# Kernel tuning notes

Measured on AMD Instinct MI355X. Metric: run time of the kernel, lower is better.

The kernel has to match this reference:

```python
import jax, jax.numpy as jnp
import numpy as np

MAX_LENGTH = 25
SOS_TOKEN = 0


def setup_inputs() -> dict:
    key = jax.random.key(0)
    B, S, H, V = 32, 50, 256, 50257
    ks = jax.random.split(key, 16)
    u = lambda k, shape, fan: jax.random.uniform(k, shape, jnp.float32, -1.0, 1.0) / np.sqrt(fan)
    return {
        "encoder_hidden": jax.random.normal(ks[0], (1, B, H), jnp.float32),
        "encoder_outputs": jax.random.normal(ks[1], (B, S, H), jnp.float32),
        "target_tensor": jax.random.randint(ks[2], (B, MAX_LENGTH), 0, V),
        "embedding": jax.random.normal(ks[3], (V, H), jnp.float32) * 0.02,
        "Wa_w": u(ks[4], (H, H), H), "Wa_b": u(ks[5], (H,), H),
        "Ua_w": u(ks[6], (H, H), H), "Ua_b": u(ks[7], (H,), H),
        "Va_w": u(ks[8], (1, H), H), "Va_b": u(ks[9], (1,), H),
        "gru_w_ih": u(ks[10], (3 * H, 2 * H), H), "gru_b_ih": u(ks[11], (3 * H,), H),
        "gru_w_hh": u(ks[12], (3 * H, H), H), "gru_b_hh": u(ks[13], (3 * H,), H),
        "out_w": u(ks[14], (V, H), H), "out_b": u(ks[15], (V,), H),
    }


def reference(encoder_hidden, encoder_outputs, target_tensor, embedding,
              Wa_w, Wa_b, Ua_w, Ua_b, Va_w, Va_b,
              gru_w_ih, gru_b_ih, gru_w_hh, gru_b_hh, out_w, out_b):
    B, S, H = encoder_outputs.shape
    keys = encoder_outputs
    # Ua(keys) is step-invariant: precompute.  [B,S,H]
    ua_keys = jnp.einsum("bsh,gh->bsg", keys, Ua_w) + Ua_b
    # teacher-forced input tokens: [SOS, target[:, :-1]] -> [T,B]
    toks = jnp.concatenate(
        [jnp.full((B, 1), SOS_TOKEN, dtype=target_tensor.dtype),
         target_tensor[:, : MAX_LENGTH - 1]], axis=1).T

    def step(h, tok):
        # h: [B,H], tok: [B]
        emb = embedding[tok]                                   # [B,H]
        # Bahdanau attention (dropout is identity in eval mode)
        wa_q = h @ Wa_w.T + Wa_b                               # [B,H]
        e = jnp.tanh(wa_q[:, None, :] + ua_keys)               # [B,S,H]
        scores = jnp.einsum("bsh,h->bs", e, Va_w[0]) + Va_b[0]  # [B,S]
        w = jax.nn.softmax(scores, axis=-1)                    # [B,S]
        ctx = jnp.einsum("bs,bsh->bh", w, keys)                # [B,H]
        # GRU cell (PyTorch gate order: r, z, n)
        x = jnp.concatenate([emb, ctx], axis=-1)               # [B,2H]
        gi = x @ gru_w_ih.T + gru_b_ih                         # [B,3H]
        gh = h @ gru_w_hh.T + gru_b_hh                         # [B,3H]
        ir, iz, inn = jnp.split(gi, 3, axis=-1)
        hr, hz, hn = jnp.split(gh, 3, axis=-1)
        r = jax.nn.sigmoid(ir + hr)
        z = jax.nn.sigmoid(iz + hz)
        n = jnp.tanh(inn + r * hn)
        h2 = (1.0 - z) * n + z * h
        logits = h2 @ out_w.T + out_b                          # [B,V]
        return h2, (logits, w)

    h0 = encoder_hidden[0]                                     # [B,H]
    hT, (logits, attn) = jax.lax.scan(step, h0, toks)          # [T,B,V], [T,B,S]
    dec_out = jax.nn.log_softmax(logits.transpose(1, 0, 2), axis=-1)  # [B,T,V]
    attentions = attn.transpose(1, 0, 2)                       # [B,T,S]
    return dec_out, hT[None], attentions
```

## Files before the change

kernel.cpp:

```cpp
#include <hip/hip_runtime.h>
#include <math.h>

#define B_ 32
#define S_ 50
#define H_ 256
#define T_ 25
#define V_ 50257
#define VP 50260
#define NCH 786
#define NROW (B_ * T_)
#define NWROW 1024
#define VT_ 3144
#define MROW 54
#define SOS 0

typedef unsigned short ushort_t;
typedef __attribute__((ext_vector_type(8))) unsigned short ushort8;
typedef __attribute__((ext_vector_type(8))) short short8v;
typedef __attribute__((ext_vector_type(4))) float f32x4;

__device__ ushort_t g_ua[B_ * S_ * H_];
__device__ ushort_t g_hbf[NROW * H_];
__device__ float    g_gie[T_ * B_ * 3 * H_];
__device__ ushort_t g_wpk[(size_t)VT_ * 32 * 16 * 8];
__device__ ushort_t g_wcat[NWROW * H_];
__device__ ushort_t g_MT2[B_ * 768 * MROW];
__device__ ushort_t g_lgt[(size_t)NROW * VP];
__device__ float    g_pmax[NROW * NCH];
__device__ float    g_psum[NROW * NCH];

__device__ __forceinline__ float bf2f(ushort_t h) {
  union { unsigned int u; float f; } c; c.u = ((unsigned int)h) << 16; return c.f;
}
__device__ __forceinline__ ushort_t f2bf(float f) {
  union { float f; unsigned int u; } c; c.f = f;
  unsigned int u = c.u;
  return (ushort_t)((u + 0x7FFFu + ((u >> 16) & 1u)) >> 16);
}
__device__ __forceinline__ float tanh_fast(float x) {
  const float e = __expf(2.f * x);
  return 1.f - 2.f / (e + 1.f);
}

__global__ void k_pre(const float* __restrict__ keys, const float* __restrict__ Ua_w,
                      const float* __restrict__ Ua_b, const float* __restrict__ Wa_b,
                      const float* __restrict__ W_hh, const float* __restrict__ Wa_w,
                      const float* __restrict__ W_ih, const float* __restrict__ b_ih,
                      const int* __restrict__ tgt, const float* __restrict__ emb_tab) {
  __shared__ float sbuf[S_ * H_];
  const int bid = blockIdx.x, tid = threadIdx.x;

  if (bid < B_ * S_) {
    sbuf[tid] = keys[bid * H_ + tid];
    sbuf[H_ + tid] = Ua_b[tid] + Wa_b[tid];
    __syncthreads();
    const int sub = tid & 15, grp = tid >> 4;
#pragma unroll 4
    for (int it = 0; it < 16; ++it) {
      const int row = it * 16 + grp;
      const float4* wr = (const float4*)(Ua_w + (size_t)row * H_);
      float a = 0.f;
#pragma unroll
      for (int st = 0; st < 4; ++st) {
        const float4 w = wr[st * 16 + sub];
        const float4 x = *(const float4*)(sbuf + st * 64 + sub * 4);
        a += w.x * x.x + w.y * x.y + w.z * x.z + w.w * x.w;
      }
      a += __shfl_xor(a, 8); a += __shfl_xor(a, 4);
      a += __shfl_xor(a, 2); a += __shfl_xor(a, 1);
      if (sub == 0) g_ua[(size_t)bid * H_ + row] = f2bf(a + sbuf[H_ + row]);
    }
  } else if (bid < 1984) {
    const int cc = bid - 1600;
    const int c = cc % 12, b = cc / 12;
    {
      const float4* src = (const float4*)(keys + (size_t)b * S_ * H_);
      float4* dst = (float4*)sbuf;
      for (int i = tid; i < S_ * H_ / 4; i += 256) dst[i] = src[i];
    }
    __syncthreads();
    const int sub = tid & 15, grp = tid >> 4;
#pragma unroll 1
    for (int it = 0; it < 4; ++it) {
      const int j = c * 64 + it * 16 + grp;
      float w16[16];
#pragma unroll
      for (int kp = 0; kp < 16; ++kp)
        w16[kp] = W_ih[(size_t)j * (2 * H_) + H_ + sub + 16 * kp];
#pragma unroll 1
      for (int s = 0; s < S_; ++s) {
        float a = 0.f;
#pragma unroll
        for (int kp = 0; kp < 16; ++kp) a += w16[kp] * sbuf[s * H_ + sub + 16 * kp];
        a += __shfl_xor(a, 8); a += __shfl_xor(a, 4);
        a += __shfl_xor(a, 2); a += __shfl_xor(a, 1);
        if (sub == 0) g_MT2[(size_t)b * 768 * MROW + j * MROW + s] = f2bf(a);
      }
    }
  } else if (bid < 2284) {
    const int cc = bid - 1984;
    const int chunk = cc % 12, t = cc / 12;
    for (int i = tid; i < B_ * H_; i += 256) {
      const int b = i >> 8, g = i & 255;
      const int tok = (t == 0) ? SOS : tgt[b * T_ + (t - 1)];
      sbuf[i] = emb_tab[(size_t)tok * H_ + g];
    }
    __syncthreads();
    const int vl = tid & 63, wd = tid >> 6;
    const int j = chunk * 64 + vl;
    const float4* wrow = (const float4*)(W_ih + (size_t)j * (2 * H_));
    const float4* se4 = (const float4*)sbuf;
    float acc[8];
    const float base = b_ih[j];
#pragma unroll
    for (int bb = 0; bb < 8; ++bb) acc[bb] = base;
    for (int k4 = 0; k4 < 64; ++k4) {
      const float4 w = wrow[k4];
#pragma unroll
      for (int bb = 0; bb < 8; ++bb) {
        const float4 x = se4[(wd * 8 + bb) * 64 + k4];
        acc[bb] += w.x * x.x + w.y * x.y + w.z * x.z + w.w * x.w;
      }
    }
#pragma unroll
    for (int bb = 0; bb < 8; ++bb)
      g_gie[((size_t)t * B_ + (wd * 8 + bb)) * (3 * H_) + j] = acc[bb];
  } else {
    const size_t i0 = (size_t)(bid - 2284) * 256 + tid;
    for (size_t i = i0; i < (size_t)NWROW * H_; i += 256u * 256u) {
      const int r = (int)(i >> 8), k = (int)(i & 255);
      const float v = (r < 256) ? Wa_w[r * H_ + k] : W_hh[(r - 256) * H_ + k];
      g_wcat[i] = f2bf(v);
    }
  }
}

__global__ void __launch_bounds__(1024, 1)
k_recur(const float* __restrict__ enc_h, const float* __restrict__ Va_w,
        const float* __restrict__ Va_b, const float* __restrict__ b_hh,
        const float* __restrict__ out_w, float* __restrict__ out) {
  __shared__ ushort_t s_ua[S_ * H_];
  __shared__ ushort_t s_M[768 * MROW];
  __shared__ float s_res[NWROW];
  __shared__ float s_mw[768];
  __shared__ float s_h[H_];
  __shared__ float s_va[H_];
  __shared__ float s_score[64], s_w[64];
  const int bidx = blockIdx.x, tid = threadIdx.x;

  if (bidx >= 32) {
    const size_t total = (size_t)VT_ * 32 * 16;
    for (size_t p = (size_t)(bidx - 32) * 1024 + tid; p < total;
         p += (size_t)(gridDim.x - 32) * 1024) {
      const int c = (int)(p & 15);
      const int kg = (int)((p >> 4) & 31);
      const int vt = (int)(p >> 9);
      const int v = vt * 16 + c;
      short8v val = {0, 0, 0, 0, 0, 0, 0, 0};
      if (v < V_) {
        const float4* owr = (const float4*)(out_w + (size_t)v * H_ + kg * 8);
        const float4 f0 = owr[0], f1 = owr[1];
        val[0] = (short)f2bf(f0.x); val[1] = (short)f2bf(f0.y);
        val[2] = (short)f2bf(f0.z); val[3] = (short)f2bf(f0.w);
        val[4] = (short)f2bf(f1.x); val[5] = (short)f2bf(f1.y);
        val[6] = (short)f2bf(f1.z); val[7] = (short)f2bf(f1.w);
      }
      ((short8v*)g_wpk)[p] = val;
    }
    return;
  }

  const int b = bidx;
  const int lane = tid & 63, wid = tid >> 6;
  const int sub = lane & 15;
  const int grp = tid >> 4;

  {
    const uint4* src = (const uint4*)(g_ua + (size_t)b * S_ * H_);
    uint4* dst = (uint4*)s_ua;
    for (int i = tid; i < S_ * H_ / 8; i += 1024) dst[i] = src[i];
    const uint4* src2 = (const uint4*)(g_MT2 + (size_t)b * 768 * MROW);
    uint4* dst2 = (uint4*)s_M;
    for (int i = tid; i < 768 * MROW / 8; i += 1024) dst2[i] = src2[i];
  }
  float hreg = 0.f, bhh0 = 0.f, bhh1 = 0.f, bhh2 = 0.f;
  if (tid < H_) {
    hreg = enc_h[b * H_ + tid];
    s_h[tid] = hreg;
    s_va[tid] = Va_w[tid];
    bhh0 = b_hh[tid]; bhh1 = b_hh[H_ + tid]; bhh2 = b_hh[2 * H_ + tid];
  }
  if (tid >= 50 && tid < 64) s_w[tid] = 0.f;
  const float vab = Va_b[0];
  __syncthreads();

  for (int t = 0; t < T_; ++t) {
    float gie0 = 0.f, gie1 = 0.f, gie2 = 0.f;
    if (tid < H_) {
      const float* gp = g_gie + ((size_t)t * B_ + b) * (3 * H_);
      gie0 = gp[tid]; gie1 = gp[H_ + tid]; gie2 = gp[2 * H_ + tid];
    }

#pragma unroll 4
    for (int it = 0; it < 16; ++it) {
      const int row = it * 64 + grp;
      const ushort8* wr = (const ushort8*)(g_wcat + (size_t)row * H_);
      const ushort8 w0 = wr[sub], w1 = wr[16 + sub];
      const float* v0 = s_h + sub * 8;
      const float* v1 = s_h + 128 + sub * 8;
      float a0 = 0.f, a1 = 0.f;
#pragma unroll
      for (int j = 0; j < 8; ++j) { a0 += bf2f(w0[j]) * v0[j]; a1 += bf2f(w1[j]) * v1[j]; }
      float a = a0 + a1;
      a += __shfl_xor(a, 8); a += __shfl_xor(a, 4);
      a += __shfl_xor(a, 2); a += __shfl_xor(a, 1);
      if (sub == 0) s_res[row] = a;
    }
    __syncthreads();

    for (int s = wid; s < S_; s += 16) {
      const ushort_t* uarow = s_ua + s * H_;
      float acc = 0.f;
#pragma unroll
      for (int i = 0; i < 4; ++i) {
        const int gg = lane + i * 64;
        acc += tanh_fast(s_res[gg] + bf2f(uarow[gg])) * s_va[gg];
      }
      for (int off = 32; off > 0; off >>= 1) acc += __shfl_xor(acc, off);
      if (lane == 0) s_score[s] = acc + vab;
    }
    __syncthreads();

    if (tid < 64) {
      const float v = (tid < S_) ? s_score[tid] : -INFINITY;
      float m = v;
      for (int off = 32; off > 0; off >>= 1) m = fmaxf(m, __shfl_xor(m, off));
      const float e = (tid < S_) ? __expf(v - m) : 0.f;
      float ssum = e;
      for (int off = 32; off > 0; off >>= 1) ssum += __shfl_xor(ssum, off);
      const float w = e / ssum;
      if (tid < S_) {
        s_w[tid] = w;
        out[(size_t)B_ * T_ * V_ + (size_t)B_ * H_ + (size_t)(b * T_ + t) * S_ + tid] = w;
      }
    }
    __syncthreads();

    if (tid < 768) {
      const unsigned int* m32 = (const unsigned int*)s_M + tid * (MROW / 2);
      float acc = 0.f;
#pragma unroll
      for (int i = 0; i < 25; ++i) {
        const unsigned int mv = m32[i];
        acc += bf2f((ushort_t)(mv & 0xffffu)) * s_w[2 * i];
        acc += bf2f((ushort_t)(mv >> 16)) * s_w[2 * i + 1];
      }
      s_mw[tid] = acc;
    }
    __syncthreads();

    if (tid < H_) {
      const float gi0 = gie0 + s_mw[tid];
      const float gi1 = gie1 + s_mw[H_ + tid];
      const float gi2 = gie2 + s_mw[2 * H_ + tid];
      const float gh0 = s_res[256 + tid] + bhh0;
      const float gh1 = s_res[512 + tid] + bhh1;
      const float gh2 = s_res[768 + tid] + bhh2;
      const float r = 1.f / (1.f + __expf(-(gi0 + gh0)));
      const float z = 1.f / (1.f + __expf(-(gi1 + gh1)));
      const float n = tanh_fast(gi2 + r * gh2);
      const float h2 = (1.f - z) * n + z * hreg;
      hreg = h2;
      s_h[tid] = h2;
      g_hbf[((size_t)b * T_ + t) * H_ + tid] = f2bf(h2);
      if (t == T_ - 1) out[(size_t)B_ * T_ * V_ + b * H_ + tid] = h2;
    }
    __syncthreads();
  }
}

__global__ void __launch_bounds__(512, 1)
k_logits(const float* __restrict__ out_b) {
  __shared__ ushort_t sA[128 * 256];
  __shared__ ushort_t sB[128 * 256];
  const int tid = threadIdx.x, nb = blockIdx.x;
  const int n0 = nb * 128;
  const int lane = tid & 63, wv = tid >> 6;
  const int wm = wv >> 1, wn = wv & 1;
  const int l16 = lane & 15, l4 = lane >> 4;

  {
    const short8v* src = (const short8v*)g_wpk + (size_t)nb * 4096;
    short8v* dst = (short8v*)sB;
    for (int i = tid; i < 4096; i += 512) dst[i] = src[i];
  }

  int vcol[4]; float bias[4]; bool valid[4];
#pragma unroll
  for (int ni = 0; ni < 4; ++ni) {
    vcol[ni] = n0 + wn * 64 + ni * 16 + l16;
    valid[ni] = (vcol[ni] < V_);
    bias[ni] = valid[ni] ? out_b[vcol[ni]] : 0.f;
  }
  const int chunk = nb * 2 + wn;

#pragma unroll 1
  for (int mt = 0; mt < 7; ++mt) {
    const int m0 = mt * 128;
    __syncthreads();
    for (int i = tid; i < 128 * 32; i += 512) {
      const int row = i >> 5, ks = i & 31;
      const int m = m0 + row;
      ushort8 val;
      if (m < NROW) val = ((const ushort8*)(g_hbf + (size_t)m * H_))[ks];
      else { ushort8 z = {0, 0, 0, 0, 0, 0, 0, 0}; val = z; }
      *(ushort8*)((char*)sA + row * 512 + ((ks ^ (row & 7)) << 4)) = val;
    }
    __syncthreads();

    f32x4 acc[2][4];
#pragma unroll
    for (int mi = 0; mi < 2; ++mi)
#pragma unroll
      for (int ni = 0; ni < 4; ++ni) acc[mi][ni] = (f32x4){0.f, 0.f, 0.f, 0.f};

#pragma unroll 1
    for (int kk = 0; kk < 8; ++kk) {
      short8v a[2], bfr[4];
#pragma unroll
      for (int mi = 0; mi < 2; ++mi) {
        const int row = wm * 32 + mi * 16 + l16;
        const int ks = kk * 4 + l4;
        a[mi] = *(const short8v*)((const char*)sA + row * 512 + ((ks ^ (row & 7)) << 4));
      }
#pragma unroll
      for (int ni = 0; ni < 4; ++ni)
        bfr[ni] = ((const short8v*)sB)[(((wn * 4 + ni) * 32) + kk * 4 + l4) * 16 + l16];
#pragma unroll
      for (int mi = 0; mi < 2; ++mi)
#pragma unroll
        for (int ni = 0; ni < 4; ++ni)
          acc[mi][ni] = __builtin_amdgcn_mfma_f32_16x16x32_bf16(a[mi], bfr[ni], acc[mi][ni], 0, 0, 0);
    }

#pragma unroll
    for (int mi = 0; mi < 2; ++mi) {
#pragma unroll
      for (int j = 0; j < 4; ++j) {
        const int m = m0 + wm * 32 + mi * 16 + l4 * 4 + j;
        float vv[4];
        float mx = -INFINITY;
#pragma unroll
        for (int ni = 0; ni < 4; ++ni) {
          vv[ni] = acc[mi][ni][j] + bias[ni];
          if (valid[ni]) mx = fmaxf(mx, vv[ni]);
        }
        mx = fmaxf(mx, __shfl_xor(mx, 1)); mx = fmaxf(mx, __shfl_xor(mx, 2));
        mx = fmaxf(mx, __shfl_xor(mx, 4)); mx = fmaxf(mx, __shfl_xor(mx, 8));
        float es = 0.f;
#pragma unroll
        for (int ni = 0; ni < 4; ++ni) if (valid[ni]) es += __expf(vv[ni] - mx);
        es += __shfl_xor(es, 1); es += __shfl_xor(es, 2);
        es += __shfl_xor(es, 4); es += __shfl_xor(es, 8);
        if (m < NROW) {
#pragma unroll
          for (int ni = 0; ni < 4; ++ni)
            if (valid[ni]) g_lgt[(size_t)m * VP + vcol[ni]] = f2bf(vv[ni]);
          if (l16 == 0) {
            g_pmax[(size_t)m * NCH + chunk] = mx;
            g_psum[(size_t)m * NCH + chunk] = es;
          }
        }
      }
    }
  }
}

__global__ void k_wlse(float* __restrict__ out) {
  __shared__ float red[4];
  const int r = blockIdx.x;
  const int tid = threadIdx.x;
  float m = -INFINITY;
  for (int i = tid; i < NCH; i += 256) m = fmaxf(m, g_pmax[(size_t)r * NCH + i]);
  for (int off = 32; off > 0; off >>= 1) m = fmaxf(m, __shfl_xor(m, off));
  if ((tid & 63) == 0) red[tid >> 6] = m;
  __syncthreads();
  m = fmaxf(fmaxf(red[0], red[1]), fmaxf(red[2], red[3]));
  __syncthreads();
  float s = 0.f;
  for (int i = tid; i < NCH; i += 256)
    s += g_psum[(size_t)r * NCH + i] * __expf(g_pmax[(size_t)r * NCH + i] - m);
  for (int off = 32; off > 0; off >>= 1) s += __shfl_xor(s, off);
  if ((tid & 63) == 0) red[tid >> 6] = s;
  __syncthreads();
  s = red[0] + red[1] + red[2] + red[3];
  float lse = m + logf(s);
  if (!isfinite(lse)) lse = 0.f;
  const size_t obase = (size_t)r * V_;
  const unsigned int* row32 = (const unsigned int*)(g_lgt + (size_t)r * VP);
#pragma unroll 1
  for (int i = tid; i < V_ / 2; i += 256) {
    const unsigned int u = row32[i];
    out[obase + 2 * i]     = bf2f((ushort_t)(u & 0xffffu)) - lse;
    out[obase + 2 * i + 1] = bf2f((ushort_t)(u >> 16)) - lse;
  }
  if (tid == 0)
    out[obase + V_ - 1] = bf2f(g_lgt[(size_t)r * VP + V_ - 1]) - lse;
}

extern "C" void kernel_launch(void* const* d_in, const int* in_sizes, int n_in,
                              void* d_out, int out_size, void* d_ws, size_t ws_size,
                              hipStream_t stream) {
  const float* enc_h  = (const float*)d_in[0];
  const float* keys   = (const float*)d_in[1];
  const int*   tgt    = (const int*)d_in[2];
  const float* emb    = (const float*)d_in[3];
  const float* Wa_w   = (const float*)d_in[4];
  const float* Wa_b   = (const float*)d_in[5];
  const float* Ua_w   = (const float*)d_in[6];
  const float* Ua_b   = (const float*)d_in[7];
  const float* Va_w   = (const float*)d_in[8];
  const float* Va_b   = (const float*)d_in[9];
  const float* W_ih   = (const float*)d_in[10];
  const float* b_ih   = (const float*)d_in[11];
  const float* W_hh   = (const float*)d_in[12];
  const float* b_hh   = (const float*)d_in[13];
  const float* out_w  = (const float*)d_in[14];
  const float* out_b  = (const float*)d_in[15];
  float* out = (float*)d_out;
  (void)d_ws; (void)ws_size;

  hipLaunchKernelGGL(k_pre, dim3(2540), dim3(256), 0, stream,
                     keys, Ua_w, Ua_b, Wa_b, W_hh, Wa_w, W_ih, b_ih, tgt, emb);
  hipLaunchKernelGGL(k_recur, dim3(32 + 1792), dim3(1024), 0, stream,
                     enc_h, Va_w, Va_b, b_hh, out_w, out);
  hipLaunchKernelGGL(k_logits, dim3(393), dim3(512), 0, stream, out_b);
  hipLaunchKernelGGL(k_wlse, dim3(NROW), dim3(256), 0, stream, out);
}
```

Measured before the change: 493.7 us.

## Compute Ua(keys) projection with bf16 MFMA tiled GEMM in preprocessing kernel

Replaces the per-row scalar dot-product blocks (1600 blocks) for the Ua(keys) projection with 26 blocks that each compute a 128x128 tile using bf16 MFMA 16x16x32. Keys are staged in LDS with an XOR swizzle and the Ua weights are converted to bf16 on the fly. The intent is to cut the cost and block count of the preprocessing kernel. Inputs are now rounded to bf16 before the multiply, so accuracy is slightly lower, and the preprocessing kernel is a small part of the total time.

```diff
diff --git a/kernel.cpp b/kernel.cpp
--- a/kernel.cpp
+++ b/kernel.cpp
@@ -47,31 +47,85 @@
                       const float* __restrict__ W_hh, const float* __restrict__ Wa_w,
                       const float* __restrict__ W_ih, const float* __restrict__ b_ih,
                       const int* __restrict__ tgt, const float* __restrict__ emb_tab) {
-  __shared__ float sbuf[S_ * H_];
+  __shared__ float sbuf[16384];
   const int bid = blockIdx.x, tid = threadIdx.x;
 
-  if (bid < B_ * S_) {
-    sbuf[tid] = keys[bid * H_ + tid];
-    sbuf[H_ + tid] = Ua_b[tid] + Wa_b[tid];
-    __syncthreads();
-    const int sub = tid & 15, grp = tid >> 4;
-#pragma unroll 4
-    for (int it = 0; it < 16; ++it) {
-      const int row = it * 16 + grp;
-      const float4* wr = (const float4*)(Ua_w + (size_t)row * H_);
-      float a = 0.f;
-#pragma unroll
-      for (int st = 0; st < 4; ++st) {
-        const float4 w = wr[st * 16 + sub];
-        const float4 x = *(const float4*)(sbuf + st * 64 + sub * 4);
-        a += w.x * x.x + w.y * x.y + w.z * x.z + w.w * x.w;
-      }
-      a += __shfl_xor(a, 8); a += __shfl_xor(a, 4);
-      a += __shfl_xor(a, 2); a += __shfl_xor(a, 1);
-      if (sub == 0) g_ua[(size_t)bid * H_ + row] = f2bf(a + sbuf[H_ + row]);
-    }
-  } else if (bid < 1984) {
-    const int cc = bid - 1600;
+  if (bid < 26) {
+    ushort_t* sA = (ushort_t*)sbuf;
+    const int bx = bid & 1, by = bid >> 1;
+    const int n0 = bx * 128, m0 = by * 128;
+    const int lane = tid & 63, wv = tid >> 6;
+    const int wm = wv >> 1, wn = wv & 1;
+    const int l16 = lane & 15, l4 = lane >> 4;
+
+    for (int i = tid; i < 128 * 32; i += 256) {
+      const int row = i >> 5, ks = i & 31;
+      const int m = m0 + row;
+      ushort8 val = {0, 0, 0, 0, 0, 0, 0, 0};
+      if (m < B_ * S_) {
+        const float4* kr = (const float4*)(keys + (size_t)m * H_ + ks * 8);
+        const float4 f0 = kr[0], f1 = kr[1];
+        val[0] = f2bf(f0.x); val[1] = f2bf(f0.y); val[2] = f2bf(f0.z); val[3] = f2bf(f0.w);
+        val[4] = f2bf(f1.x); val[5] = f2bf(f1.y); val[6] = f2bf(f1.z); val[7] = f2bf(f1.w);
+      }
+      *(ushort8*)((char*)sA + row * 512 + ((ks ^ (row & 7)) << 4)) = val;
+    }
+    __syncthreads();
+
+    f32x4 acc[4][4];
+#pragma unroll
+    for (int mi = 0; mi < 4; ++mi)
+#pragma unroll
+      for (int ni = 0; ni < 4; ++ni) acc[mi][ni] = (f32x4){0.f, 0.f, 0.f, 0.f};
+
+#pragma unroll 1
+    for (int kk = 0; kk < 8; ++kk) {
+      short8v a[4], bfr[4];
+#pragma unroll
+      for (int mi = 0; mi < 4; ++mi) {
+        const int row = wm * 64 + mi * 16 + l16;
+        const int ks = kk * 4 + l4;
+        a[mi] = *(const short8v*)((const char*)sA + row * 512 + ((ks ^ (row & 7)) << 4));
+      }
+#pragma unroll
+      for (int ni = 0; ni < 4; ++ni) {
+        const int g = n0 + wn * 64 + ni * 16 + l16;
+        const float4* wr = (const float4*)(Ua_w + (size_t)g * H_ + kk * 32 + l4 * 8);
+        const float4 f0 = wr[0], f1 = wr[1];
+        short8v bv;
+        bv[0] = (short)f2bf(f0.x); bv[1] = (short)f2bf(f0.y);
+        bv[2] = (short)f2bf(f0.z); bv[3] = (short)f2bf(f0.w);
+        bv[4] = (short)f2bf(f1.x); bv[5] = (short)f2bf(f1.y);
+        bv[6] = (short)f2bf(f1.z); bv[7] = (short)f2bf(f1.w);
+        bfr[ni] = bv;
+      }
+#pragma unroll
+      for (int mi = 0; mi < 4; ++mi)
+#pragma unroll
+        for (int ni = 0; ni < 4; ++ni)
+          acc[mi][ni] = __builtin_amdgcn_mfma_f32_16x16x32_bf16(a[mi], bfr[ni], acc[mi][ni], 0, 0, 0);
+    }
+
+    int col[4]; float bias[4];
+#pragma unroll
+    for (int ni = 0; ni < 4; ++ni) {
+      col[ni] = n0 + wn * 64 + ni * 16 + l16;
+      bias[ni] = Ua_b[col[ni]] + Wa_b[col[ni]];
+    }
+#pragma unroll
+    for (int mi = 0; mi < 4; ++mi) {
+#pragma unroll
+      for (int j = 0; j < 4; ++j) {
+        const int m = m0 + wm * 64 + mi * 16 + l4 * 4 + j;
+        if (m < B_ * S_) {
+#pragma unroll
+          for (int ni = 0; ni < 4; ++ni)
+            g_ua[(size_t)m * H_ + col[ni]] = f2bf(acc[mi][ni][j] + bias[ni]);
+        }
+      }
+    }
+  } else if (bid < 410) {
+    const int cc = bid - 26;
     const int c = cc % 12, b = cc / 12;
     {
       const float4* src = (const float4*)(keys + (size_t)b * S_ * H_);
@@ -97,8 +151,8 @@
         if (sub == 0) g_MT2[(size_t)b * 768 * MROW + j * MROW + s] = f2bf(a);
       }
     }
-  } else if (bid < 2284) {
-    const int cc = bid - 1984;
+  } else if (bid < 710) {
+    const int cc = bid - 410;
     const int chunk = cc % 12, t = cc / 12;
     for (int i = tid; i < B_ * H_; i += 256) {
       const int b = i >> 8, g = i & 255;
@@ -126,7 +180,7 @@
     for (int bb = 0; bb < 8; ++bb)
       g_gie[((size_t)t * B_ + (wd * 8 + bb)) * (3 * H_) + j] = acc[bb];
   } else {
-    const size_t i0 = (size_t)(bid - 2284) * 256 + tid;
+    const size_t i0 = (size_t)(bid - 710) * 256 + tid;
     for (size_t i = i0; i < (size_t)NWROW * H_; i += 256u * 256u) {
       const int r = (int)(i >> 8), k = (int)(i & 255);
       const float v = (r < 256) ? Wa_w[r * H_ + k] : W_hh[(r - 256) * H_ + k];
@@ -430,7 +484,7 @@
   float* out = (float*)d_out;
   (void)d_ws; (void)ws_size;
 
-  hipLaunchKernelGGL(k_pre, dim3(2540), dim3(256), 0, stream,
+  hipLaunchKernelGGL(k_pre, dim3(966), dim3(256), 0, stream,
                      keys, Ua_w, Ua_b, Wa_b, W_hh, Wa_w, W_ih, b_ih, tgt, emb);
   hipLaunchKernelGGL(k_recur, dim3(32 + 1792), dim3(1024), 0, stream,
                      enc_h, Va_w, Va_b, b_hh, out_w, out);
```

New measurement: 487.0 us. About the same (-1.4%).
